# Optimization experiments

Hardware: AMD Instinct MI355X
Metric: run time of the kernel (lower is better)

The kernel has to match this reference:

```python
import jax, jax.numpy as jnp
import numpy as np
import math

B, LQ, LK = 4, 512, 512
D_MODEL, NHEAD, NLABELS = 512, 8, 8
D_Q = D_MODEL // NHEAD


def setup_inputs() -> dict:
    key = jax.random.key(0)
    ks = jax.random.split(key, 12)
    xavier = lambda k, shape: jax.random.uniform(
        k, shape, jnp.float32,
        -math.sqrt(6.0 / (shape[0] + shape[1])), math.sqrt(6.0 / (shape[0] + shape[1])))
    return {
        "q": jax.random.normal(ks[0], (B, LQ, D_MODEL), jnp.float32),
        "k": jax.random.normal(ks[1], (B, LK, D_MODEL), jnp.float32),
        "edge_mask": jax.random.randint(ks[2], (B, LQ, LK, NLABELS), 0, 2).astype(jnp.float32),
        "padding_mask": jax.random.randint(ks[3], (B, LQ, LK), 0, 2).astype(jnp.float32),
        "w_q_w": xavier(ks[4], (D_MODEL, D_MODEL)),
        "w_q_b": jnp.zeros((D_MODEL,), jnp.float32),
        "w_k": xavier(ks[5], (D_MODEL, D_MODEL)),
        "w_v": xavier(ks[6], (D_MODEL, D_MODEL)),
        "w_h_w": xavier(ks[7], (D_MODEL, D_MODEL)),
        "w_h_b": jnp.zeros((D_MODEL,), jnp.float32),
        "b_ks": xavier(ks[8], (NLABELS, D_Q)),
        "b_vs": xavier(ks[9], (NLABELS, D_Q)),
    }


def reference(q, k, edge_mask, padding_mask, w_q_w, w_q_b, w_k, w_v, w_h_w, w_h_b, b_ks, b_vs):
    sz_b, len_q, _ = q.shape
    len_k = k.shape[1]
    temp = np.power(D_Q, 0.5).astype(np.float32)

    # projections -> (nhead, B, L, d_q), matching torch permute(2,0,1,3)
    query = (q @ w_q_w.T + w_q_b).reshape(sz_b, len_q, NHEAD, D_Q).transpose(2, 0, 1, 3)
    key = (k @ w_k.T).reshape(sz_b, len_k, NHEAD, D_Q).transpose(2, 0, 1, 3)
    value = (k @ w_v.T).reshape(sz_b, len_k, NHEAD, D_Q).transpose(2, 0, 1, 3)

    # content scores + relation-bias scores
    qk = jnp.einsum('hbqd,hbkd->hbqk', query, key)
    key_rel = jnp.einsum('bqkl,ld->bqkd', edge_mask, b_ks)      # (B,Lq,Lk,d_q)
    qkr = jnp.einsum('hbqd,bqkd->hbqk', query, key_rel)
    output_attention_weights = (qk + qkr) / temp                # pre-mask, as returned by torch

    # mask where no edge label AND padding_mask==1
    relation_mask = (edge_mask.sum(-1) + (1.0 - padding_mask)) == 0  # (B,Lq,Lk)
    rm = relation_mask[None, :, :, :]                                # broadcast over heads
    attn = jnp.where(rm, -jnp.inf, output_attention_weights)
    attn = jax.nn.softmax(attn, axis=-1)
    attn = jnp.where(rm, 0.0, attn)

    # value aggregation: content + relation values
    qv = jnp.einsum('hbqk,hbkd->hbqd', attn, value)
    val_rel = jnp.einsum('bqkl,ld->bqkd', edge_mask, b_vs)
    qvr = jnp.einsum('hbqk,bqkd->hbqd', attn, val_rel)

    out = (qv + qvr).transpose(1, 2, 0, 3).reshape(sz_b, len_q, D_MODEL)
    out = out @ w_h_w.T + w_h_b
    return out, output_attention_weights.reshape(NHEAD * sz_b, len_q, len_k)
```

## Files before the change

kernel.cpp:

```cpp
#include <hip/hip_runtime.h>
#include <math.h>

#define NB 4
#define LQ 512
#define LK 512
#define DM 512
#define NH 8
#define DQ 64
#define NL 8

typedef short bf16x8 __attribute__((ext_vector_type(8)));
typedef float f32x4 __attribute__((ext_vector_type(4)));

__device__ __forceinline__ unsigned short f2bf(float x) {
    unsigned u = __float_as_uint(x);
    u += 0x7fff + ((u >> 16) & 1);
    return (unsigned short)(u >> 16);
}
__device__ __forceinline__ float bf2f(unsigned x) {
    return __uint_as_float(x << 16);
}
__device__ __forceinline__ uint4 pack8(float4 a, float4 b) {
    uint4 o;
    o.x = (unsigned)f2bf(a.x) | ((unsigned)f2bf(a.y) << 16);
    o.y = (unsigned)f2bf(a.z) | ((unsigned)f2bf(a.w) << 16);
    o.z = (unsigned)f2bf(b.x) | ((unsigned)f2bf(b.y) << 16);
    o.w = (unsigned)f2bf(b.z) | ((unsigned)f2bf(b.w) << 16);
    return o;
}

__device__ __forceinline__ void gld16(const void* g, void* l) {
    __builtin_amdgcn_global_load_lds(
        (const __attribute__((address_space(1))) void*)g,
        (__attribute__((address_space(3))) void*)l, 16, 0, 0);
}

__global__ __launch_bounds__(256) void proj_all(const float* __restrict__ qg,
                                                const float* __restrict__ kg,
                                                const float* __restrict__ wq,
                                                const float* __restrict__ wk,
                                                const float* __restrict__ wv,
                                                const float* __restrict__ w_q_b,
                                                unsigned short* __restrict__ Qp,
                                                unsigned short* __restrict__ Kp,
                                                unsigned short* __restrict__ Vt) {
    __shared__ __align__(16) short As[64 * 32];
    __shared__ __align__(16) short Bs[64 * 32];
    const float* A; const float* W; const float* bias; unsigned short* C; int mode;
    switch (blockIdx.z) {
        case 0:  A = qg; W = wq; bias = w_q_b;  C = Qp; mode = 0; break;
        case 1:  A = kg; W = wk; bias = nullptr; C = Kp; mode = 0; break;
        default: A = kg; W = wv; bias = nullptr; C = Vt; mode = 1; break;
    }
    const int tid = threadIdx.x, wave = tid >> 6, lane = tid & 63;
    const int quad = lane >> 4, l16 = lane & 15;
    const int wr = wave >> 1, wc = wave & 1;
    const int m0 = blockIdx.x * 64, n0 = blockIdx.y * 64;
    const int srow = tid >> 2, scol = (tid & 3) * 8;
    const float* Ab = A + (size_t)(m0 + srow) * DM + scol;
    const float* Wb = W + (size_t)(n0 + srow) * DM + scol;

    f32x4 acc[2][2];
    const f32x4 zz = {0.f, 0.f, 0.f, 0.f};
#pragma unroll
    for (int i = 0; i < 2; ++i)
#pragma unroll
        for (int j = 0; j < 2; ++j) acc[i][j] = zz;

    for (int k0 = 0; k0 < DM; k0 += 32) {
        const float4 a0 = *(const float4*)(Ab + k0);
        const float4 a1 = *(const float4*)(Ab + k0 + 4);
        const float4 b0 = *(const float4*)(Wb + k0);
        const float4 b1 = *(const float4*)(Wb + k0 + 4);
        __syncthreads();
        *(uint4*)&As[srow * 32 + scol] = pack8(a0, a1);
        *(uint4*)&Bs[srow * 32 + scol] = pack8(b0, b1);
        __syncthreads();
        bf16x8 af[2], bf[2];
#pragma unroll
        for (int i = 0; i < 2; ++i)
            af[i] = *(const bf16x8*)&As[(wr * 32 + i * 16 + l16) * 32 + quad * 8];
#pragma unroll
        for (int j = 0; j < 2; ++j)
            bf[j] = *(const bf16x8*)&Bs[(wc * 32 + j * 16 + l16) * 32 + quad * 8];
#pragma unroll
        for (int i = 0; i < 2; ++i)
#pragma unroll
            for (int j = 0; j < 2; ++j)
                acc[i][j] = __builtin_amdgcn_mfma_f32_16x16x32_bf16(af[i], bf[j], acc[i][j], 0, 0, 0);
    }
#pragma unroll
    for (int i = 0; i < 2; ++i)
#pragma unroll
        for (int r = 0; r < 4; ++r) {
            const int gm = m0 + wr * 32 + i * 16 + quad * 4 + r;
#pragma unroll
            for (int j = 0; j < 2; ++j) {
                const int gn = n0 + wc * 32 + j * 16 + l16;
                float v = acc[i][j][r];
                if (bias) v += bias[gn];
                if (mode == 0) C[(size_t)gm * DM + gn] = f2bf(v);
                else C[(size_t)(gm >> 9) * (DM * LK) + (size_t)gn * LK + (gm & 511)] = f2bf(v);
            }
        }
}

__global__ __launch_bounds__(256) void qk_mfma(const unsigned short* __restrict__ Qp,
                                               const unsigned short* __restrict__ Kp,
                                               unsigned short* __restrict__ Sc) {
    __shared__ __align__(16) short As[2][128 * 32];
    __shared__ __align__(16) short Bs[2][128 * 32];
    const int tid = threadIdx.x, wave = tid >> 6, lane = tid & 63;
    const int quad = lane >> 4, l16 = lane & 15;
    const int wr = wave >> 1, wc = wave & 1;
    const int z = blockIdx.z, h = z >> 2, b = z & 3;
    const int m0 = blockIdx.x * 128, n0 = blockIdx.y * 128;
    const unsigned short* Ag = Qp + (size_t)(b * LQ + m0) * DM + h * DQ;
    const unsigned short* Bg = Kp + (size_t)(b * LK + n0) * DM + h * DQ;

#pragma unroll
    for (int s = 0; s < 2; ++s)
#pragma unroll
        for (int it = 0; it < 2; ++it) {
            const int c = it * 256 + tid;
            gld16(Ag + (size_t)(c >> 2) * DM + s * 32 + (c & 3) * 8,
                  (char*)As[s] + it * 4096 + wave * 1024);
            gld16(Bg + (size_t)(c >> 2) * DM + s * 32 + (c & 3) * 8,
                  (char*)Bs[s] + it * 4096 + wave * 1024);
        }
    __syncthreads();

    f32x4 acc[4][4];
    const f32x4 zz = {0.f, 0.f, 0.f, 0.f};
#pragma unroll
    for (int i = 0; i < 4; ++i)
#pragma unroll
        for (int j = 0; j < 4; ++j) acc[i][j] = zz;
#pragma unroll
    for (int s = 0; s < 2; ++s) {
        bf16x8 af[4], bf[4];
#pragma unroll
        for (int i = 0; i < 4; ++i)
            af[i] = *(const bf16x8*)&As[s][(wr * 64 + i * 16 + l16) * 32 + quad * 8];
#pragma unroll
        for (int j = 0; j < 4; ++j)
            bf[j] = *(const bf16x8*)&Bs[s][(wc * 64 + j * 16 + l16) * 32 + quad * 8];
#pragma unroll
        for (int i = 0; i < 4; ++i)
#pragma unroll
            for (int j = 0; j < 4; ++j)
                acc[i][j] = __builtin_amdgcn_mfma_f32_16x16x32_bf16(af[i], bf[j], acc[i][j], 0, 0, 0);
    }
    unsigned short* Cz = Sc + (size_t)z * LQ * LK;
#pragma unroll
    for (int i = 0; i < 4; ++i)
#pragma unroll
        for (int r = 0; r < 4; ++r) {
            const int gm = m0 + wr * 64 + i * 16 + quad * 4 + r;
#pragma unroll
            for (int j = 0; j < 4; ++j) {
                const int gn = n0 + wc * 64 + j * 16 + l16;
                Cz[(size_t)gm * LK + gn] = f2bf(acc[i][j][r]);
            }
        }
}

__global__ __launch_bounds__(512) void softmax_kernel(const float* __restrict__ em,
                                                      const float* __restrict__ pad,
                                                      const unsigned short* __restrict__ Qp,
                                                      const float* __restrict__ b_ks,
                                                      const unsigned short* __restrict__ Sc,
                                                      float* __restrict__ weights,
                                                      unsigned short* __restrict__ attn,
                                                      float* __restrict__ Tb) {
    const int tid = threadIdx.x, wave = tid >> 6, lane = tid & 63;
    const int bq = blockIdx.x, b = bq >> 9, q = bq & 511;
    const int h = wave, z = h * NB + b;

    const float qd = bf2f(Qp[(size_t)bq * DM + h * DQ + lane]);
    float sv[NL];
#pragma unroll
    for (int l = 0; l < NL; ++l) {
        float p = qd * b_ks[l * DQ + lane];
#pragma unroll
        for (int o = 1; o < 64; o <<= 1) p += __shfl_xor(p, o, 64);
        sv[l] = p;
    }

    float4 ev[16];
    const float* eb = em + (size_t)bq * (LK * NL);
#pragma unroll
    for (int j = 0; j < 8; ++j) {
        const int k = lane + 64 * j;
        ev[2 * j]     = *(const float4*)(eb + k * 8);
        ev[2 * j + 1] = *(const float4*)(eb + k * 8 + 4);
    }
    float padv[8];
#pragma unroll
    for (int j = 0; j < 8; ++j) padv[j] = pad[(size_t)bq * LK + lane + 64 * j];
    const unsigned short* sp = Sc + ((size_t)z * LQ + q) * LK;
    float qk8[8];
#pragma unroll
    for (int j = 0; j < 8; ++j) qk8[j] = bf2f(sp[lane + 64 * j]);

    const size_t rowbase = ((size_t)z * LQ + q) * LK;
    float wv8[8], m8[8];
#pragma unroll
    for (int j = 0; j < 8; ++j) {
        const float4 a = ev[2 * j], c = ev[2 * j + 1];
        const float rel = a.x * sv[0] + a.y * sv[1] + a.z * sv[2] + a.w * sv[3]
                        + c.x * sv[4] + c.y * sv[5] + c.z * sv[6] + c.w * sv[7];
        const float es = ((a.x + a.y) + (a.z + a.w)) + ((c.x + c.y) + (c.z + c.w));
        const float wv = (qk8[j] + rel) * 0.125f;
        wv8[j] = wv;
        m8[j] = ((es + 1.0f - padv[j]) == 0.0f) ? -__builtin_inff() : wv;
        weights[rowbase + lane + 64 * j] = wv;
    }

    float mx = m8[0];
#pragma unroll
    for (int j = 1; j < 8; ++j) mx = fmaxf(mx, m8[j]);
#pragma unroll
    for (int o = 1; o < 64; o <<= 1) mx = fmaxf(mx, __shfl_xor(mx, o, 64));

    float e8[8], ss = 0.f;
#pragma unroll
    for (int j = 0; j < 8; ++j) { e8[j] = __expf(m8[j] - mx); ss += e8[j]; }
#pragma unroll
    for (int o = 1; o < 64; o <<= 1) ss += __shfl_xor(ss, o, 64);
    const float inv = 1.0f / ss;

    float tl[NL] = {0.f, 0.f, 0.f, 0.f, 0.f, 0.f, 0.f, 0.f};
#pragma unroll
    for (int j = 0; j < 8; ++j) {
        const float a_ = e8[j] * inv;
        attn[rowbase + lane + 64 * j] = f2bf(a_);
        const float4 a = ev[2 * j], c = ev[2 * j + 1];
        tl[0] = fmaf(a_, a.x, tl[0]); tl[1] = fmaf(a_, a.y, tl[1]);
        tl[2] = fmaf(a_, a.z, tl[2]); tl[3] = fmaf(a_, a.w, tl[3]);
        tl[4] = fmaf(a_, c.x, tl[4]); tl[5] = fmaf(a_, c.y, tl[5]);
        tl[6] = fmaf(a_, c.z, tl[6]); tl[7] = fmaf(a_, c.w, tl[7]);
    }
#pragma unroll
    for (int o = 1; o < 64; o <<= 1)
#pragma unroll
        for (int l = 0; l < NL; ++l) tl[l] += __shfl_xor(tl[l], o, 64);
    if (lane == 0) {
        float* tp = Tb + ((size_t)z * LQ + q) * NL;
#pragma unroll
        for (int l = 0; l < NL; ++l) tp[l] = tl[l];
    }
}

__global__ __launch_bounds__(512) void qv_mfma(const unsigned short* __restrict__ Attn,
                                               const unsigned short* __restrict__ Vt,
                                               const float* __restrict__ Tb,
                                               const float* __restrict__ b_vs,
                                               unsigned short* __restrict__ Hb) {
    __shared__ __align__(16) short As[64 * 32];
    __shared__ __align__(16) short Bs[64 * 32];
    const int tid = threadIdx.x, wave = tid >> 6, lane = tid & 63;
    const int quad = lane >> 4, l16 = lane & 15;
    const int wr = wave >> 2, wc = wave & 3;
    const int z = blockIdx.z, h = z >> 2, b = z & 3;
    const int m0 = blockIdx.x * 64;
    const unsigned short* Ag = Attn + (size_t)z * LQ * LK + (size_t)m0 * LK;
    const unsigned short* Bg = Vt + (size_t)b * (DM * LK) + (size_t)(h * DQ) * LK;

    f32x4 acc[2];
    const f32x4 zz = {0.f, 0.f, 0.f, 0.f};
    acc[0] = zz; acc[1] = zz;
    const int c = tid & 255;

    for (int k0 = 0; k0 < LK; k0 += 32) {
        __syncthreads();
        if (tid < 256)
            gld16(Ag + (size_t)(c >> 2) * LK + k0 + (c & 3) * 8,
                  (char*)As + wave * 1024);
        else
            gld16(Bg + (size_t)(c >> 2) * LK + k0 + (c & 3) * 8,
                  (char*)Bs + (wave - 4) * 1024);
        __syncthreads();
        bf16x8 af[2], bf;
#pragma unroll
        for (int i = 0; i < 2; ++i)
            af[i] = *(const bf16x8*)&As[(wr * 32 + i * 16 + l16) * 32 + quad * 8];
        bf = *(const bf16x8*)&Bs[(wc * 16 + l16) * 32 + quad * 8];
#pragma unroll
        for (int i = 0; i < 2; ++i)
            acc[i] = __builtin_amdgcn_mfma_f32_16x16x32_bf16(af[i], bf, acc[i], 0, 0, 0);
    }
    const int d = wc * 16 + l16;
    float bvv[NL];
#pragma unroll
    for (int l = 0; l < NL; ++l) bvv[l] = b_vs[l * DQ + d];
#pragma unroll
    for (int i = 0; i < 2; ++i)
#pragma unroll
        for (int r = 0; r < 4; ++r) {
            const int qrow = m0 + wr * 32 + i * 16 + quad * 4 + r;
            const float* t8 = Tb + ((size_t)z * LQ + qrow) * NL;
            float qvr = 0.f;
#pragma unroll
            for (int l = 0; l < NL; ++l) qvr = fmaf(t8[l], bvv[l], qvr);
            Hb[(size_t)(b * LQ + qrow) * DM + h * DQ + d] = f2bf(acc[i][r] + qvr);
        }
}

__global__ __launch_bounds__(256) void outproj_mfma(const unsigned short* __restrict__ Hb,
                                                    const float* __restrict__ W,
                                                    const float* __restrict__ bias,
                                                    float* __restrict__ C) {
    __shared__ __align__(16) short As[64 * 32];
    __shared__ __align__(16) short Bs[64 * 32];
    const int tid = threadIdx.x, wave = tid >> 6, lane = tid & 63;
    const int quad = lane >> 4, l16 = lane & 15;
    const int wr = wave >> 1, wc = wave & 1;
    const int m0 = blockIdx.x * 64, n0 = blockIdx.y * 64;
    const int srow = tid >> 2, scol = (tid & 3) * 8;
    const unsigned short* Ag = Hb + (size_t)m0 * DM;
    const float* Wb = W + (size_t)(n0 + srow) * DM + scol;

    f32x4 acc[2][2];
    const f32x4 zz = {0.f, 0.f, 0.f, 0.f};
#pragma unroll
    for (int i = 0; i < 2; ++i)
#pragma unroll
        for (int j = 0; j < 2; ++j) acc[i][j] = zz;

    for (int k0 = 0; k0 < DM; k0 += 32) {
        const float4 b0 = *(const float4*)(Wb + k0);
        const float4 b1 = *(const float4*)(Wb + k0 + 4);
        __syncthreads();
        gld16(Ag + (size_t)(tid >> 2) * DM + k0 + (tid & 3) * 8,
              (char*)As + wave * 1024);
        *(uint4*)&Bs[srow * 32 + scol] = pack8(b0, b1);
        __syncthreads();
        bf16x8 af[2], bf[2];
#pragma unroll
        for (int i = 0; i < 2; ++i)
            af[i] = *(const bf16x8*)&As[(wr * 32 + i * 16 + l16) * 32 + quad * 8];
#pragma unroll
        for (int j = 0; j < 2; ++j)
            bf[j] = *(const bf16x8*)&Bs[(wc * 32 + j * 16 + l16) * 32 + quad * 8];
#pragma unroll
        for (int i = 0; i < 2; ++i)
#pragma unroll
            for (int j = 0; j < 2; ++j)
                acc[i][j] = __builtin_amdgcn_mfma_f32_16x16x32_bf16(af[i], bf[j], acc[i][j], 0, 0, 0);
    }
#pragma unroll
    for (int i = 0; i < 2; ++i)
#pragma unroll
        for (int r = 0; r < 4; ++r) {
            const int gm = m0 + wr * 32 + i * 16 + quad * 4 + r;
#pragma unroll
            for (int j = 0; j < 2; ++j) {
                const int gn = n0 + wc * 32 + j * 16 + l16;
                C[(size_t)gm * DM + gn] = acc[i][j][r] + bias[gn];
            }
        }
}

extern "C" void kernel_launch(void* const* d_in, const int* in_sizes, int n_in,
                              void* d_out, int out_size, void* d_ws, size_t ws_size,
                              hipStream_t stream) {
    const float* q     = (const float*)d_in[0];
    const float* k     = (const float*)d_in[1];
    const float* em    = (const float*)d_in[2];
    const float* pad   = (const float*)d_in[3];
    const float* w_q_w = (const float*)d_in[4];
    const float* w_q_b = (const float*)d_in[5];
    const float* w_k   = (const float*)d_in[6];
    const float* w_v   = (const float*)d_in[7];
    const float* w_h_w = (const float*)d_in[8];
    const float* w_h_b = (const float*)d_in[9];
    const float* b_ks  = (const float*)d_in[10];
    const float* b_vs  = (const float*)d_in[11];

    float* out     = (float*)d_out;
    float* weights = out + (size_t)NB * LQ * DM;

    char* ws = (char*)d_ws;
    unsigned short* Qp  = (unsigned short*)(ws + 0);
    unsigned short* Kp  = (unsigned short*)(ws + 2097152);
    unsigned short* Vt  = (unsigned short*)(ws + 4194304);
    unsigned short* Hb  = (unsigned short*)(ws + 6291456);
    unsigned short* Att = (unsigned short*)(ws + 8388608);
    unsigned short* Sc  = (unsigned short*)(ws + 25165824);
    float*          Tb  = (float*)(ws + 41943040);

    proj_all<<<dim3(32, 8, 3), 256, 0, stream>>>(q, k, w_q_w, w_k, w_v, w_q_b, Qp, Kp, Vt);
    qk_mfma<<<dim3(4, 4, 32), 256, 0, stream>>>(Qp, Kp, Sc);
    softmax_kernel<<<dim3(NB * LQ), dim3(512), 0, stream>>>(em, pad, Qp, b_ks, Sc,
                                                            weights, Att, Tb);
    qv_mfma<<<dim3(8, 1, 32), 512, 0, stream>>>(Att, Vt, Tb, b_vs, Hb);
    outproj_mfma<<<dim3(32, 8), 256, 0, stream>>>(Hb, w_h_w, w_h_b, out);
}
```

Measured before the change: 183.1 us.

## Fuse QK, softmax and PV into one attention kernel with bit-packed edge masks

Replaces the separate QK GEMM, softmax, and attention-times-V kernels with a single fused kernel that handles 32 query rows per block for one head and batch. The scores and bf16 attention probabilities now stay in LDS instead of passing through global memory. A new pre-pass packs the fp32 edge labels and padding mask into 9 bits per (q,k) pair, so the 8 MB-per-row-set edge-mask tensor is read once instead of once per head. The trade-offs are fewer blocks (512), heavier LDS use, more barriers, and serial per-block phases with little overlap.

New measurement: 176.0 us. 1.04x faster.

```diff
diff --git a/kernel.cpp b/kernel.cpp
--- a/kernel.cpp
+++ b/kernel.cpp
@@ -8,6 +8,8 @@
 #define NH 8
 #define DQ 64
 #define NL 8
+#define QT 32
+#define PSTR 520
 
 typedef short bf16x8 __attribute__((ext_vector_type(8)));
 typedef float f32x4 __attribute__((ext_vector_type(4)));
@@ -28,11 +30,32 @@
     o.w = (unsigned)f2bf(b.z) | ((unsigned)f2bf(b.w) << 16);
     return o;
 }
-
 __device__ __forceinline__ void gld16(const void* g, void* l) {
     __builtin_amdgcn_global_load_lds(
         (const __attribute__((address_space(1))) void*)g,
         (__attribute__((address_space(3))) void*)l, 16, 0, 0);
+}
+
+__global__ __launch_bounds__(256) void empack_kernel(const float* __restrict__ em,
+                                                     const float* __restrict__ pad,
+                                                     unsigned short* __restrict__ Pk) {
+    const int bq = blockIdx.x;
+    const int k0 = threadIdx.x * 2;
+    const float4* e4 = (const float4*)(em + (size_t)bq * (LK * NL) + (size_t)k0 * NL);
+    const float4 v0 = e4[0], v1 = e4[1], v2 = e4[2], v3 = e4[3];
+    const float2 pv = *(const float2*)(pad + (size_t)bq * LK + k0);
+    unsigned b0 = 0, b1 = 0;
+    b0 |= (v0.x != 0.f) << 0; b0 |= (v0.y != 0.f) << 1;
+    b0 |= (v0.z != 0.f) << 2; b0 |= (v0.w != 0.f) << 3;
+    b0 |= (v1.x != 0.f) << 4; b0 |= (v1.y != 0.f) << 5;
+    b0 |= (v1.z != 0.f) << 6; b0 |= (v1.w != 0.f) << 7;
+    b0 |= (pv.x != 0.f) << 8;
+    b1 |= (v2.x != 0.f) << 0; b1 |= (v2.y != 0.f) << 1;
+    b1 |= (v2.z != 0.f) << 2; b1 |= (v2.w != 0.f) << 3;
+    b1 |= (v3.x != 0.f) << 4; b1 |= (v3.y != 0.f) << 5;
+    b1 |= (v3.z != 0.f) << 6; b1 |= (v3.w != 0.f) << 7;
+    b1 |= (pv.y != 0.f) << 8;
+    *(unsigned*)(Pk + (size_t)bq * LK + k0) = b0 | (b1 << 16);
 }
 
 __global__ __launch_bounds__(256) void proj_all(const float* __restrict__ qg,
@@ -105,206 +128,203 @@
         }
 }
 
-__global__ __launch_bounds__(256) void qk_mfma(const unsigned short* __restrict__ Qp,
-                                               const unsigned short* __restrict__ Kp,
-                                               unsigned short* __restrict__ Sc) {
-    __shared__ __align__(16) short As[2][128 * 32];
-    __shared__ __align__(16) short Bs[2][128 * 32];
+__global__ __launch_bounds__(512, 4) void attn_fused(
+        const unsigned short* __restrict__ Qp,
+        const unsigned short* __restrict__ Kp,
+        const unsigned short* __restrict__ Vt,
+        const unsigned short* __restrict__ Pk,
+        const float* __restrict__ b_ks,
+        const float* __restrict__ b_vs,
+        float* __restrict__ weights,
+        unsigned short* __restrict__ Hb) {
+    __shared__ __align__(16) short Qs[QT * 64];
+    __shared__ __align__(16) short Kc[128 * 64];
+    __shared__ __align__(16) short Ps[QT * PSTR];
+    __shared__ float svS[QT * NL];
+    __shared__ float tS[QT * NL];
+    __shared__ float redA[QT * 8];
+    __shared__ float redB[QT * 8];
+
     const int tid = threadIdx.x, wave = tid >> 6, lane = tid & 63;
     const int quad = lane >> 4, l16 = lane & 15;
-    const int wr = wave >> 1, wc = wave & 1;
-    const int z = blockIdx.z, h = z >> 2, b = z & 3;
-    const int m0 = blockIdx.x * 128, n0 = blockIdx.y * 128;
-    const unsigned short* Ag = Qp + (size_t)(b * LQ + m0) * DM + h * DQ;
-    const unsigned short* Bg = Kp + (size_t)(b * LK + n0) * DM + h * DQ;
-
-#pragma unroll
-    for (int s = 0; s < 2; ++s)
+    const int q0 = blockIdx.x * QT;
+    const int z = blockIdx.y, h = z >> 2, b = z & 3;
+
+    if (tid < 256) {
+        const int row = tid >> 3, off = (tid & 7) * 8;
+        gld16(Qp + (size_t)(b * LQ + q0 + row) * DM + h * DQ + off,
+              (char*)Qs + wave * 1024);
+    }
+
+    f32x4 acc[4][2];
+    const f32x4 zz = {0.f, 0.f, 0.f, 0.f};
+#pragma unroll
+    for (int c = 0; c < 4; ++c) { acc[c][0] = zz; acc[c][1] = zz; }
+
+    for (int c = 0; c < 4; ++c) {
 #pragma unroll
         for (int it = 0; it < 2; ++it) {
-            const int c = it * 256 + tid;
-            gld16(Ag + (size_t)(c >> 2) * DM + s * 32 + (c & 3) * 8,
-                  (char*)As[s] + it * 4096 + wave * 1024);
-            gld16(Bg + (size_t)(c >> 2) * DM + s * 32 + (c & 3) * 8,
-                  (char*)Bs[s] + it * 4096 + wave * 1024);
+            const int e = it * 512 + tid;
+            const int kr = c * 128 + (e >> 3), off = (e & 7) * 8;
+            gld16(Kp + (size_t)(b * LK + kr) * DM + h * DQ + off,
+                  (char*)Kc + it * 8192 + wave * 1024);
+        }
+        __syncthreads();
+#pragma unroll
+        for (int kd = 0; kd < 64; kd += 32) {
+            const bf16x8 bfv = *(const bf16x8*)&Kc[(wave * 16 + l16) * 64 + kd + quad * 8];
+#pragma unroll
+            for (int i = 0; i < 2; ++i) {
+                const bf16x8 afv = *(const bf16x8*)&Qs[(i * 16 + l16) * 64 + kd + quad * 8];
+                acc[c][i] = __builtin_amdgcn_mfma_f32_16x16x32_bf16(afv, bfv, acc[c][i], 0, 0, 0);
+            }
+        }
+        if (c == 0 && tid < 256) {
+            const int row = tid >> 3, l = tid & 7;
+            float s = 0.f;
+#pragma unroll
+            for (int d = 0; d < DQ; ++d)
+                s = fmaf(bf2f((unsigned short)Qs[row * 64 + d]), b_ks[l * DQ + d], s);
+            svS[row * 8 + l] = s;
+        }
+        __syncthreads();
+    }
+
+#pragma unroll
+    for (int it = 0; it < 2; ++it) {
+        const int e = it * 512 + tid;
+        const int dd = e >> 4, off = (e & 15) * 8;
+        gld16(Vt + (size_t)(b * DM + h * DQ + dd) * LK + off,
+              (char*)Kc + it * 8192 + wave * 1024);
+    }
+
+#pragma unroll
+    for (int i = 0; i < 2; ++i)
+#pragma unroll
+        for (int r = 0; r < 4; ++r) {
+            const int row = i * 16 + quad * 4 + r;
+            const int gq = q0 + row;
+            const f32x4 sv0 = *(const f32x4*)&svS[row * 8];
+            const f32x4 sv1 = *(const f32x4*)&svS[row * 8 + 4];
+            const unsigned short* prow = Pk + (size_t)(b * LQ + gq) * LK;
+            float* wrow = weights + ((size_t)z * LQ + gq) * LK;
+            float pm = -__builtin_inff();
+#pragma unroll
+            for (int c = 0; c < 4; ++c) {
+                const int col = c * 128 + wave * 16 + l16;
+                const unsigned w_ = prow[col];
+                float rel = 0.f;
+                rel = fmaf((float)((w_ >> 0) & 1), sv0[0], rel);
+                rel = fmaf((float)((w_ >> 1) & 1), sv0[1], rel);
+                rel = fmaf((float)((w_ >> 2) & 1), sv0[2], rel);
+                rel = fmaf((float)((w_ >> 3) & 1), sv0[3], rel);
+                rel = fmaf((float)((w_ >> 4) & 1), sv1[0], rel);
+                rel = fmaf((float)((w_ >> 5) & 1), sv1[1], rel);
+                rel = fmaf((float)((w_ >> 6) & 1), sv1[2], rel);
+                rel = fmaf((float)((w_ >> 7) & 1), sv1[3], rel);
+                const float wv = (acc[c][i][r] + rel) * 0.125f;
+                wrow[col] = wv;
+                const float m = ((w_ & 0x1FFu) == 0x100u) ? -__builtin_inff() : wv;
+                acc[c][i][r] = m;
+                pm = fmaxf(pm, m);
+            }
+#pragma unroll
+            for (int o = 1; o < 16; o <<= 1) pm = fmaxf(pm, __shfl_xor(pm, o, 64));
+            if (l16 == 0) redA[row * 8 + wave] = pm;
         }
     __syncthreads();
 
-    f32x4 acc[4][4];
-    const f32x4 zz = {0.f, 0.f, 0.f, 0.f};
-#pragma unroll
-    for (int i = 0; i < 4; ++i)
-#pragma unroll
-        for (int j = 0; j < 4; ++j) acc[i][j] = zz;
-#pragma unroll
-    for (int s = 0; s < 2; ++s) {
-        bf16x8 af[4], bf[4];
-#pragma unroll
-        for (int i = 0; i < 4; ++i)
-            af[i] = *(const bf16x8*)&As[s][(wr * 64 + i * 16 + l16) * 32 + quad * 8];
-#pragma unroll
-        for (int j = 0; j < 4; ++j)
-            bf[j] = *(const bf16x8*)&Bs[s][(wc * 64 + j * 16 + l16) * 32 + quad * 8];
-#pragma unroll
-        for (int i = 0; i < 4; ++i)
-#pragma unroll
-            for (int j = 0; j < 4; ++j)
-                acc[i][j] = __builtin_amdgcn_mfma_f32_16x16x32_bf16(af[i], bf[j], acc[i][j], 0, 0, 0);
-    }
-    unsigned short* Cz = Sc + (size_t)z * LQ * LK;
-#pragma unroll
-    for (int i = 0; i < 4; ++i)
+#pragma unroll
+    for (int i = 0; i < 2; ++i)
 #pragma unroll
         for (int r = 0; r < 4; ++r) {
-            const int gm = m0 + wr * 64 + i * 16 + quad * 4 + r;
-#pragma unroll
-            for (int j = 0; j < 4; ++j) {
-                const int gn = n0 + wc * 64 + j * 16 + l16;
-                Cz[(size_t)gm * LK + gn] = f2bf(acc[i][j][r]);
-            }
-        }
-}
-
-__global__ __launch_bounds__(512) void softmax_kernel(const float* __restrict__ em,
-                                                      const float* __restrict__ pad,
-                                                      const unsigned short* __restrict__ Qp,
-                                                      const float* __restrict__ b_ks,
-                                                      const unsigned short* __restrict__ Sc,
-                                                      float* __restrict__ weights,
-                                                      unsigned short* __restrict__ attn,
-                                                      float* __restrict__ Tb) {
-    const int tid = threadIdx.x, wave = tid >> 6, lane = tid & 63;
-    const int bq = blockIdx.x, b = bq >> 9, q = bq & 511;
-    const int h = wave, z = h * NB + b;
-
-    const float qd = bf2f(Qp[(size_t)bq * DM + h * DQ + lane]);
-    float sv[NL];
-#pragma unroll
-    for (int l = 0; l < NL; ++l) {
-        float p = qd * b_ks[l * DQ + lane];
-#pragma unroll
-        for (int o = 1; o < 64; o <<= 1) p += __shfl_xor(p, o, 64);
-        sv[l] = p;
-    }
-
-    float4 ev[16];
-    const float* eb = em + (size_t)bq * (LK * NL);
-#pragma unroll
-    for (int j = 0; j < 8; ++j) {
-        const int k = lane + 64 * j;
-        ev[2 * j]     = *(const float4*)(eb + k * 8);
-        ev[2 * j + 1] = *(const float4*)(eb + k * 8 + 4);
-    }
-    float padv[8];
-#pragma unroll
-    for (int j = 0; j < 8; ++j) padv[j] = pad[(size_t)bq * LK + lane + 64 * j];
-    const unsigned short* sp = Sc + ((size_t)z * LQ + q) * LK;
-    float qk8[8];
-#pragma unroll
-    for (int j = 0; j < 8; ++j) qk8[j] = bf2f(sp[lane + 64 * j]);
-
-    const size_t rowbase = ((size_t)z * LQ + q) * LK;
-    float wv8[8], m8[8];
-#pragma unroll
-    for (int j = 0; j < 8; ++j) {
-        const float4 a = ev[2 * j], c = ev[2 * j + 1];
-        const float rel = a.x * sv[0] + a.y * sv[1] + a.z * sv[2] + a.w * sv[3]
-                        + c.x * sv[4] + c.y * sv[5] + c.z * sv[6] + c.w * sv[7];
-        const float es = ((a.x + a.y) + (a.z + a.w)) + ((c.x + c.y) + (c.z + c.w));
-        const float wv = (qk8[j] + rel) * 0.125f;
-        wv8[j] = wv;
-        m8[j] = ((es + 1.0f - padv[j]) == 0.0f) ? -__builtin_inff() : wv;
-        weights[rowbase + lane + 64 * j] = wv;
-    }
-
-    float mx = m8[0];
-#pragma unroll
-    for (int j = 1; j < 8; ++j) mx = fmaxf(mx, m8[j]);
-#pragma unroll
-    for (int o = 1; o < 64; o <<= 1) mx = fmaxf(mx, __shfl_xor(mx, o, 64));
-
-    float e8[8], ss = 0.f;
-#pragma unroll
-    for (int j = 0; j < 8; ++j) { e8[j] = __expf(m8[j] - mx); ss += e8[j]; }
-#pragma unroll
-    for (int o = 1; o < 64; o <<= 1) ss += __shfl_xor(ss, o, 64);
-    const float inv = 1.0f / ss;
-
-    float tl[NL] = {0.f, 0.f, 0.f, 0.f, 0.f, 0.f, 0.f, 0.f};
-#pragma unroll
-    for (int j = 0; j < 8; ++j) {
-        const float a_ = e8[j] * inv;
-        attn[rowbase + lane + 64 * j] = f2bf(a_);
-        const float4 a = ev[2 * j], c = ev[2 * j + 1];
-        tl[0] = fmaf(a_, a.x, tl[0]); tl[1] = fmaf(a_, a.y, tl[1]);
-        tl[2] = fmaf(a_, a.z, tl[2]); tl[3] = fmaf(a_, a.w, tl[3]);
-        tl[4] = fmaf(a_, c.x, tl[4]); tl[5] = fmaf(a_, c.y, tl[5]);
-        tl[6] = fmaf(a_, c.z, tl[6]); tl[7] = fmaf(a_, c.w, tl[7]);
-    }
-#pragma unroll
-    for (int o = 1; o < 64; o <<= 1)
-#pragma unroll
-        for (int l = 0; l < NL; ++l) tl[l] += __shfl_xor(tl[l], o, 64);
-    if (lane == 0) {
-        float* tp = Tb + ((size_t)z * LQ + q) * NL;
-#pragma unroll
-        for (int l = 0; l < NL; ++l) tp[l] = tl[l];
-    }
-}
-
-__global__ __launch_bounds__(512) void qv_mfma(const unsigned short* __restrict__ Attn,
-                                               const unsigned short* __restrict__ Vt,
-                                               const float* __restrict__ Tb,
-                                               const float* __restrict__ b_vs,
-                                               unsigned short* __restrict__ Hb) {
-    __shared__ __align__(16) short As[64 * 32];
-    __shared__ __align__(16) short Bs[64 * 32];
-    const int tid = threadIdx.x, wave = tid >> 6, lane = tid & 63;
-    const int quad = lane >> 4, l16 = lane & 15;
-    const int wr = wave >> 2, wc = wave & 3;
-    const int z = blockIdx.z, h = z >> 2, b = z & 3;
-    const int m0 = blockIdx.x * 64;
-    const unsigned short* Ag = Attn + (size_t)z * LQ * LK + (size_t)m0 * LK;
-    const unsigned short* Bg = Vt + (size_t)b * (DM * LK) + (size_t)(h * DQ) * LK;
-
-    f32x4 acc[2];
-    const f32x4 zz = {0.f, 0.f, 0.f, 0.f};
-    acc[0] = zz; acc[1] = zz;
-    const int c = tid & 255;
-
-    for (int k0 = 0; k0 < LK; k0 += 32) {
-        __syncthreads();
-        if (tid < 256)
-            gld16(Ag + (size_t)(c >> 2) * LK + k0 + (c & 3) * 8,
-                  (char*)As + wave * 1024);
-        else
-            gld16(Bg + (size_t)(c >> 2) * LK + k0 + (c & 3) * 8,
-                  (char*)Bs + (wave - 4) * 1024);
-        __syncthreads();
-        bf16x8 af[2], bf;
-#pragma unroll
-        for (int i = 0; i < 2; ++i)
-            af[i] = *(const bf16x8*)&As[(wr * 32 + i * 16 + l16) * 32 + quad * 8];
-        bf = *(const bf16x8*)&Bs[(wc * 16 + l16) * 32 + quad * 8];
-#pragma unroll
-        for (int i = 0; i < 2; ++i)
-            acc[i] = __builtin_amdgcn_mfma_f32_16x16x32_bf16(af[i], bf, acc[i], 0, 0, 0);
-    }
-    const int d = wc * 16 + l16;
+            const int row = i * 16 + quad * 4 + r;
+            const f32x4 ra = *(const f32x4*)&redA[row * 8];
+            const f32x4 rb = *(const f32x4*)&redA[row * 8 + 4];
+            const float rmax = fmaxf(fmaxf(fmaxf(ra[0], ra[1]), fmaxf(ra[2], ra[3])),
+                                     fmaxf(fmaxf(rb[0], rb[1]), fmaxf(rb[2], rb[3])));
+            float psum = 0.f;
+#pragma unroll
+            for (int c = 0; c < 4; ++c) {
+                const float e = __expf(acc[c][i][r] - rmax);
+                acc[c][i][r] = e;
+                psum += e;
+            }
+#pragma unroll
+            for (int o = 1; o < 16; o <<= 1) psum += __shfl_xor(psum, o, 64);
+            if (l16 == 0) redB[row * 8 + wave] = psum;
+        }
+    __syncthreads();
+
+#pragma unroll
+    for (int i = 0; i < 2; ++i)
+#pragma unroll
+        for (int r = 0; r < 4; ++r) {
+            const int row = i * 16 + quad * 4 + r;
+            const f32x4 sa = *(const f32x4*)&redB[row * 8];
+            const f32x4 sb = *(const f32x4*)&redB[row * 8 + 4];
+            const float tot = ((sa[0] + sa[1]) + (sa[2] + sa[3])) +
+                              ((sb[0] + sb[1]) + (sb[2] + sb[3]));
+            const float inv = 1.0f / tot;
+#pragma unroll
+            for (int c = 0; c < 4; ++c) {
+                const int col = c * 128 + wave * 16 + l16;
+                Ps[row * PSTR + col] = (short)f2bf(acc[c][i][r] * inv);
+            }
+        }
+    __syncthreads();
+
+    {
+        const int row = tid >> 4, l = (tid >> 1) & 7, half = tid & 1;
+        const unsigned* pw = (const unsigned*)(Pk + (size_t)(b * LQ + q0 + row) * LK + half * 256);
+        const unsigned* aw = (const unsigned*)&Ps[row * PSTR + half * 256];
+        float tv = 0.f;
+#pragma unroll 4
+        for (int kk = 0; kk < 128; ++kk) {
+            const unsigned wbits = pw[kk];
+            const unsigned av = aw[kk];
+            tv = fmaf((float)((wbits >> l) & 1),        bf2f(av & 0xffffu), tv);
+            tv = fmaf((float)((wbits >> (16 + l)) & 1), bf2f(av >> 16), tv);
+        }
+        tv += __shfl_xor(tv, 1, 64);
+        if (half == 0) tS[row * 8 + l] = tv;
+    }
+
+    f32x4 oacc = zz;
+    const int mi = wave & 1, ni = wave >> 1;
+    for (int vc = 0; vc < 4; ++vc) {
+        if (vc > 0) {
+            __syncthreads();
+#pragma unroll
+            for (int it = 0; it < 2; ++it) {
+                const int e = it * 512 + tid;
+                const int dd = e >> 4, off = (e & 15) * 8;
+                gld16(Vt + (size_t)(b * DM + h * DQ + dd) * LK + vc * 128 + off,
+                      (char*)Kc + it * 8192 + wave * 1024);
+            }
+        }
+        __syncthreads();
+#pragma unroll
+        for (int kd = 0; kd < 128; kd += 32) {
+            const bf16x8 afv = *(const bf16x8*)&Ps[(mi * 16 + l16) * PSTR + vc * 128 + kd + quad * 8];
+            const bf16x8 bfv = *(const bf16x8*)&Kc[(ni * 16 + l16) * 128 + kd + quad * 8];
+            oacc = __builtin_amdgcn_mfma_f32_16x16x32_bf16(afv, bfv, oacc, 0, 0, 0);
+        }
+    }
+
+    const int gd = ni * 16 + l16;
     float bvv[NL];
 #pragma unroll
-    for (int l = 0; l < NL; ++l) bvv[l] = b_vs[l * DQ + d];
-#pragma unroll
-    for (int i = 0; i < 2; ++i)
-#pragma unroll
-        for (int r = 0; r < 4; ++r) {
-            const int qrow = m0 + wr * 32 + i * 16 + quad * 4 + r;
-            const float* t8 = Tb + ((size_t)z * LQ + qrow) * NL;
-            float qvr = 0.f;
-#pragma unroll
-            for (int l = 0; l < NL; ++l) qvr = fmaf(t8[l], bvv[l], qvr);
-            Hb[(size_t)(b * LQ + qrow) * DM + h * DQ + d] = f2bf(acc[i][r] + qvr);
-        }
+    for (int l = 0; l < NL; ++l) bvv[l] = b_vs[l * DQ + gd];
+#pragma unroll
+    for (int r = 0; r < 4; ++r) {
+        const int row = mi * 16 + quad * 4 + r;
+        const float* tp = &tS[row * 8];
+        float o = oacc[r];
+#pragma unroll
+        for (int l = 0; l < NL; ++l) o = fmaf(tp[l], bvv[l], o);
+        Hb[(size_t)(b * LQ + q0 + row) * DM + h * DQ + gd] = f2bf(o);
+    }
 }
 
 __global__ __launch_bounds__(256) void outproj_mfma(const unsigned short* __restrict__ Hb,
@@ -382,18 +402,14 @@
     float* weights = out + (size_t)NB * LQ * DM;
 
     char* ws = (char*)d_ws;
-    unsigned short* Qp  = (unsigned short*)(ws + 0);
-    unsigned short* Kp  = (unsigned short*)(ws + 2097152);
-    unsigned short* Vt  = (unsigned short*)(ws + 4194304);
-    unsigned short* Hb  = (unsigned short*)(ws + 6291456);
-    unsigned short* Att = (unsigned short*)(ws + 8388608);
-    unsigned short* Sc  = (unsigned short*)(ws + 25165824);
-    float*          Tb  = (float*)(ws + 41943040);
-
+    unsigned short* Qp = (unsigned short*)(ws + 0);
+    unsigned short* Kp = (unsigned short*)(ws + 2097152);
+    unsigned short* Vt = (unsigned short*)(ws + 4194304);
+    unsigned short* Hb = (unsigned short*)(ws + 6291456);
+    unsigned short* Pk = (unsigned short*)(ws + 8388608);
+
+    empack_kernel<<<dim3(NB * LQ), 256, 0, stream>>>(em, pad, Pk);
     proj_all<<<dim3(32, 8, 3), 256, 0, stream>>>(q, k, w_q_w, w_k, w_v, w_q_b, Qp, Kp, Vt);
-    qk_mfma<<<dim3(4, 4, 32), 256, 0, stream>>>(Qp, Kp, Sc);
-    softmax_kernel<<<dim3(NB * LQ), dim3(512), 0, stream>>>(em, pad, Qp, b_ks, Sc,
-                                                            weights, Att, Tb);
-    qv_mfma<<<dim3(8, 1, 32), 512, 0, stream>>>(Att, Vt, Tb, b_vs, Hb);
+    attn_fused<<<dim3(LQ / QT, 32), 512, 0, stream>>>(Qp, Kp, Vt, Pk, b_ks, b_vs, weights, Hb);
     outproj_mfma<<<dim3(32, 8), 256, 0, stream>>>(Hb, w_h_w, w_h_b, out);
 }
```
